# Optimization experiments

Measured on AMD Instinct MI355X. Metric: run time of the kernel, lower is better.

Reference implementation:

```python
import jax, jax.numpy as jnp
import numpy as np

BATCH = 4096
FILTER_NUM = 1024
REL_CNT = 19
REL_DIM = 1024


def setup_inputs() -> dict:
    key = jax.random.key(0)
    k1, k2, k3 = jax.random.split(key, 3)
    conv_output = jax.random.normal(k1, (BATCH, FILTER_NUM, REL_CNT), dtype=jnp.float32)
    R_output = jax.random.normal(k2, (REL_CNT, REL_DIM), dtype=jnp.float32)
    # U ~ truncated_normal(stddev=0.1); plain normal*0.1 is an acceptable init stand-in
    U = jax.random.normal(k3, (FILTER_NUM, REL_DIM), dtype=jnp.float32) * 0.1
    return {"conv_output": conv_output, "R_output": R_output, "U": U}


def reference(conv_output, R_output, U):
    # Original: for each relation r, score[:, r] = conv_output[:, :, r] @ U @ R_output[r, :]
    # Batched as a single einsum: scores[b, r] = sum_{f,e} conv[b,f,r] * U[f,e] * R[r,e]
    # Contract the large f axis first (GEMM-dominant), then reduce over e per relation.
    proj = jnp.einsum('bfr,fe->bre', conv_output, U)      # [B, R, E]
    scores = jnp.einsum('bre,re->br', proj, R_output)     # [B, R]
    return scores
```

## Files before the change

### kernel.cpp

```cpp
#include <hip/hip_runtime.h>

#define BATCH      4096
#define FILTER_NUM 1024
#define REL_CNT    19
#define REL_DIM    1024

__global__ __launch_bounds__(256) void compute_V_kernel(
        const float* __restrict__ U,
        const float* __restrict__ Rm,
        float* __restrict__ V)
{
    const int f   = blockIdx.x;
    const int tid = threadIdx.x;

    float acc[REL_CNT];
#pragma unroll
    for (int r = 0; r < REL_CNT; ++r) acc[r] = 0.0f;

    const float* __restrict__ Urow = U + (size_t)f * REL_DIM;
    for (int e = tid; e < REL_DIM; e += 256) {
        const float u = Urow[e];
#pragma unroll
        for (int r = 0; r < REL_CNT; ++r)
            acc[r] = fmaf(u, Rm[r * REL_DIM + e], acc[r]);
    }

    __shared__ float s[4][REL_CNT];
    const int lane = tid & 63;
    const int wave = tid >> 6;
#pragma unroll
    for (int r = 0; r < REL_CNT; ++r) {
        float v = acc[r];
#pragma unroll
        for (int off = 32; off > 0; off >>= 1)
            v += __shfl_down(v, off, 64);
        if (lane == 0) s[wave][r] = v;
    }
    __syncthreads();
    if (tid < REL_CNT)
        V[f * REL_CNT + tid] = s[0][tid] + s[1][tid] + s[2][tid] + s[3][tid];
}

__global__ __launch_bounds__(256) void score_kernel(
        const float* __restrict__ conv,
        const float* __restrict__ V,
        float* __restrict__ out)
{
    const int b   = blockIdx.x;
    const int tid = threadIdx.x;

    const float* __restrict__ cb = conv + (size_t)b * FILTER_NUM * REL_CNT;

    float acc[REL_CNT];
#pragma unroll
    for (int r = 0; r < REL_CNT; ++r) acc[r] = 0.0f;

    for (int f = tid; f < FILTER_NUM; f += 256) {
        const float* __restrict__ c = cb + f * REL_CNT;
        const float* __restrict__ v = V  + f * REL_CNT;
#pragma unroll
        for (int r = 0; r < REL_CNT; ++r)
            acc[r] = fmaf(c[r], v[r], acc[r]);
    }

    __shared__ float s[4][REL_CNT];
    const int lane = tid & 63;
    const int wave = tid >> 6;
#pragma unroll
    for (int r = 0; r < REL_CNT; ++r) {
        float v = acc[r];
#pragma unroll
        for (int off = 32; off > 0; off >>= 1)
            v += __shfl_down(v, off, 64);
        if (lane == 0) s[wave][r] = v;
    }
    __syncthreads();
    if (tid < REL_CNT)
        out[b * REL_CNT + tid] = s[0][tid] + s[1][tid] + s[2][tid] + s[3][tid];
}

extern "C" void kernel_launch(void* const* d_in, const int* in_sizes, int n_in,
                              void* d_out, int out_size, void* d_ws, size_t ws_size,
                              hipStream_t stream) {
    const float* conv = (const float*)d_in[0];
    const float* Rm   = (const float*)d_in[1];
    const float* U    = (const float*)d_in[2];
    float*       out  = (float*)d_out;
    float*       V    = (float*)d_ws;

    compute_V_kernel<<<FILTER_NUM, 256, 0, stream>>>(U, Rm, V);
    score_kernel<<<BATCH, 256, 0, stream>>>(conv, V, out);
}
```

Before: 443.3 us.

## Coalesce score kernel loads as flat float4 stream with rotating accumulator mapping

The score kernel now treats each batch row's conv slab and V as flat contiguous arrays and reads them as float4 with fully coalesced indexing. Each element's relation index is tracked by a per-thread offset plus a compile-time rotation, using 19 accumulators. The old strided per-f loads (stride 19 floats) are replaced by unit-stride vector loads. The reduction becomes a shared-memory scatter of 256x19 partials followed by a two-level tree sum, which costs more LDS space and sync steps.

After: 429.0 us. -3.2%, faster.

```diff
diff --git a/kernel.cpp b/kernel.cpp
--- a/kernel.cpp
+++ b/kernel.cpp
@@ -4,6 +4,8 @@
 #define FILTER_NUM 1024
 #define REL_CNT    19
 #define REL_DIM    1024
+#define SLAB       (FILTER_NUM * REL_CNT)
+#define ITERS      (SLAB / (256 * 4))
 
 __global__ __launch_bounds__(256) void compute_V_kernel(
         const float* __restrict__ U,
@@ -49,34 +51,54 @@
     const int b   = blockIdx.x;
     const int tid = threadIdx.x;
 
-    const float* __restrict__ cb = conv + (size_t)b * FILTER_NUM * REL_CNT;
+    const float4* __restrict__ c4 = (const float4*)(conv + (size_t)b * SLAB);
+    const float4* __restrict__ v4 = (const float4*)V;
+
+    const int o = (4 * tid) % REL_CNT;
 
     float acc[REL_CNT];
 #pragma unroll
-    for (int r = 0; r < REL_CNT; ++r) acc[r] = 0.0f;
+    for (int j = 0; j < REL_CNT; ++j) acc[j] = 0.0f;
 
-    for (int f = tid; f < FILTER_NUM; f += 256) {
-        const float* __restrict__ c = cb + f * REL_CNT;
-        const float* __restrict__ v = V  + f * REL_CNT;
 #pragma unroll
-        for (int r = 0; r < REL_CNT; ++r)
-            acc[r] = fmaf(c[r], v[r], acc[r]);
+    for (int iter = 0; iter < ITERS; ++iter) {
+        const int idx = iter * 256 + tid;
+        const float4 c = c4[idx];
+        const float4 v = v4[idx];
+        acc[(17 * iter + 0) % REL_CNT] = fmaf(c.x, v.x, acc[(17 * iter + 0) % REL_CNT]);
+        acc[(17 * iter + 1) % REL_CNT] = fmaf(c.y, v.y, acc[(17 * iter + 1) % REL_CNT]);
+        acc[(17 * iter + 2) % REL_CNT] = fmaf(c.z, v.z, acc[(17 * iter + 2) % REL_CNT]);
+        acc[(17 * iter + 3) % REL_CNT] = fmaf(c.w, v.w, acc[(17 * iter + 3) % REL_CNT]);
     }
 
-    __shared__ float s[4][REL_CNT];
-    const int lane = tid & 63;
-    const int wave = tid >> 6;
+    __shared__ float s[256 * REL_CNT];
 #pragma unroll
-    for (int r = 0; r < REL_CNT; ++r) {
-        float v = acc[r];
-#pragma unroll
-        for (int off = 32; off > 0; off >>= 1)
-            v += __shfl_down(v, off, 64);
-        if (lane == 0) s[wave][r] = v;
+    for (int j = 0; j < REL_CNT; ++j) {
+        int r = o + j;
+        if (r >= REL_CNT) r -= REL_CNT;
+        s[tid * REL_CNT + r] = acc[j];
     }
     __syncthreads();
-    if (tid < REL_CNT)
-        out[b * REL_CNT + tid] = s[0][tid] + s[1][tid] + s[2][tid] + s[3][tid];
+
+    __shared__ float s2[8 * REL_CNT];
+    if (tid < 8 * REL_CNT) {
+        const int r = tid % REL_CNT;
+        const int g = tid / REL_CNT;
+        float sum = 0.0f;
+#pragma unroll
+        for (int i = 0; i < 32; ++i)
+            sum += s[(g * 32 + i) * REL_CNT + r];
+        s2[g * REL_CNT + r] = sum;
+    }
+    __syncthreads();
+
+    if (tid < REL_CNT) {
+        float sum = 0.0f;
+#pragma unroll
+        for (int g = 0; g < 8; ++g)
+            sum += s2[g * REL_CNT + tid];
+        out[b * REL_CNT + tid] = sum;
+    }
 }
 
 extern "C" void kernel_launch(void* const* d_in, const int* in_sizes, int n_in,
```
